# Kernel tuning notes

Hardware: AMD Instinct MI355X
Metric: run time of the kernel (lower is better)

## Reference

```python
import jax, jax.numpy as jnp
import numpy as np

B, N, S, K, R = 4, 8192, 2048, 64, 0.2  # batch, points, centroids, neighbors, ball radius
EPS = 1e-5  # BatchNorm eps


def fps_indices(x, n_samples):
    """Farthest point sampling; returns int32 [B, n_samples] indices."""
    xs = jax.lax.stop_gradient(x)
    Bb, Nn, _ = xs.shape

    def step(carry, _):
        dist, farthest = carry
        centroid = jnp.take_along_axis(xs, farthest[:, None, None], axis=1)  # [B,1,3]
        d = jnp.sum((xs - centroid) ** 2, axis=-1)  # [B,N]
        dist = jnp.minimum(dist, d)
        nxt = jnp.argmax(dist, axis=-1).astype(jnp.int32)
        return (dist, nxt), farthest

    init = (jnp.full((Bb, Nn), 1e10, xs.dtype), jnp.zeros((Bb,), jnp.int32))
    _, idxs = jax.lax.scan(step, init, None, length=n_samples)  # [S,B]
    return jnp.transpose(idxs)  # [B,S]


def ball_query(x, centroids, radius, k):
    """First k point indices within radius of each centroid, -1 padded. int32 [B,S,k]."""
    xs = jax.lax.stop_gradient(x)
    cs = jax.lax.stop_gradient(centroids)
    Nn = xs.shape[1]
    d2 = jnp.sum((cs[:, :, None, :] - xs[:, None, :, :]) ** 2, axis=-1)  # [B,S,N]
    cand = jnp.where(d2 < radius * radius, jnp.arange(Nn, dtype=jnp.int32), Nn)
    neg_topk, _ = jax.lax.top_k(-cand, k)  # k smallest candidate indices
    idx = -neg_topk
    return jnp.where(idx == Nn, -1, idx)


def _forward(x, x_complete, layers, idx_fps, idx_ball):
    centroids = jnp.take_along_axis(x, idx_fps[..., None], axis=1)  # [B,S,3]
    valid = idx_ball >= 0  # [B,S,K]
    sidx = jnp.maximum(idx_ball, 0)
    gather = lambda pts: jax.vmap(lambda p, i: p[i])(pts, sidx)  # [B,S,K,C]
    x_local = gather(x) - centroids[:, :, None, :]  # relative coords
    feats = jnp.concatenate([gather(x_complete), x_local], axis=-1)  # [B,S,K,67]
    h = feats.reshape(B, S * K, -1).transpose(0, 2, 1)  # [B,67,S*K]
    for (W, b, g, bt, m, v) in layers:  # Conv1d(k=1) -> BN(eval) -> ReLU
        h = jnp.einsum('oc,bcn->bon', W, h) + b[None, :, None]
        h = (h - m[None, :, None]) * (g * jax.lax.rsqrt(v + EPS))[None, :, None] + bt[None, :, None]
        h = jax.nn.relu(h)
    h = h.reshape(B, -1, S, K)  # [B,128,S,K]
    h = jnp.where(valid[:, None, :, :], h, -jnp.inf)  # mask invalid neighbors
    pooled = jnp.max(h, axis=3)  # masked max pool over neighborhood
    return centroids, pooled.transpose(0, 2, 1)  # [B,S,3], [B,S,128]


def setup_inputs():
    key = jax.random.key(0)
    ks = jax.random.split(key, 8)
    x = jax.random.uniform(ks[0], (B, N, 3), jnp.float32)
    x_complete = jax.random.normal(ks[1], (B, N, 64), jnp.float32)
    dims = [67, 64, 64, 128]
    inp = {'x': x, 'x_complete': x_complete}
    for i in range(3):
        cin, cout = dims[i], dims[i + 1]
        kk = jax.random.split(ks[2 + i], 6)
        inp[f'W{i+1}'] = jax.random.normal(kk[0], (cout, cin), jnp.float32) * 0.05
        inp[f'b{i+1}'] = jax.random.normal(kk[1], (cout,), jnp.float32) * 0.02
        inp[f'g{i+1}'] = 1.0 + 0.1 * jax.random.normal(kk[2], (cout,), jnp.float32)
        inp[f'bt{i+1}'] = jax.random.normal(kk[3], (cout,), jnp.float32) * 0.02
        inp[f'm{i+1}'] = jax.random.normal(kk[4], (cout,), jnp.float32) * 0.05
        inp[f'v{i+1}'] = jax.random.uniform(kk[5], (cout,), jnp.float32, minval=0.5, maxval=1.5)
    return inp


def reference(x, x_complete, W1, b1, g1, bt1, m1, v1, W2, b2, g2, bt2, m2, v2, W3, b3, g3, bt3, m3, v3):
    idx_fps = fps_indices(x, S)
    cen_sg = jnp.take_along_axis(jax.lax.stop_gradient(x), idx_fps[..., None], axis=1)
    idx_ball = ball_query(x, cen_sg, R, K)
    layers = ((W1, b1, g1, bt1, m1, v1), (W2, b2, g2, bt2, m2, v2), (W3, b3, g3, bt3, m3, v3))
    return _forward(x, x_complete, layers, idx_fps, idx_ball)
```

## Files before the change

### kernel.cpp

```cpp
#include <hip/hip_runtime.h>
#include <math.h>

#define BATCH 4
#define NPTS  8192
#define NSAMP 2048
#define KNBR  64
#define EPSF  1e-5f

typedef float v2f __attribute__((ext_vector_type(2)));

__global__ void prep_kernel(const float* __restrict__ W1, const float* __restrict__ W2,
                            const float* __restrict__ W3,
                            float* __restrict__ W1t, float* __restrict__ W2t,
                            float* __restrict__ W3t) {
    int t = threadIdx.x;
    for (int i = t; i < 64 * 67; i += 256) { int o = i / 67, c = i % 67; W1t[c * 64 + o] = W1[i]; }
    for (int i = t; i < 64 * 64; i += 256) { int o = i >> 6, c = i & 63; W2t[c * 64 + o] = W2[i]; }
    for (int i = t; i < 128 * 64; i += 256) { int o = i >> 6, c = i & 63; W3t[c * 128 + o] = W3[i]; }
}

#define DPP_FMAX(v, ctrl)                                                            \
    do {                                                                             \
        int _t = __builtin_amdgcn_update_dpp(0, __float_as_int(v), ctrl, 0xf, 0xf, true); \
        (v) = fmaxf((v), __int_as_float(_t));                                        \
    } while (0)

__global__ __launch_bounds__(256, 1) void fps_kernel(const float* __restrict__ x,
                                                     float* __restrict__ cen_out) {
#pragma clang fp contract(off)
    const int b = blockIdx.x;
    const int tid = threadIdx.x;
    const int lane = tid & 63;
    const int wid = tid >> 6;
    __shared__ float sx[NPTS], sy[NPTS], sz[NPTS];
    __shared__ __align__(16) float sd[2][4];
    __shared__ __align__(16) int   si[2][4];
    __shared__ int hist[NSAMP];

    const float* xb = x + (size_t)b * NPTS * 3;
    for (int i = tid; i < NPTS; i += 256) {
        sx[i] = xb[3 * i + 0];
        sy[i] = xb[3 * i + 1];
        sz[i] = xb[3 * i + 2];
    }
    __syncthreads();

    v2f px[16], py[16], pz[16], dist[16];
    const int base = tid * 32;
#pragma unroll
    for (int j = 0; j < 16; j++) {
        int p = base + 2 * j;
        px[j] = *(const v2f*)&sx[p];
        py[j] = *(const v2f*)&sy[p];
        pz[j] = *(const v2f*)&sz[p];
        dist[j] = (v2f){1e10f, 1e10f};
    }

    int cur = 0;
    float cx = sx[0], cy = sy[0], cz = sz[0];
    for (int s = 0; s < NSAMP; s++) {
        if (tid == 0) hist[s] = cur;
        const v2f cvx = (v2f){cx, cx}, cvy = (v2f){cy, cy}, cvz = (v2f){cz, cz};
#pragma unroll
        for (int j = 0; j < 16; j++) {
            v2f dx = px[j] - cvx;
            v2f dy = py[j] - cvy;
            v2f dz = pz[j] - cvz;
            v2f d = ((dx * dx) + (dy * dy)) + (dz * dz);
            v2f dm;
            dm.x = fminf(dist[j].x, d.x);
            dm.y = fminf(dist[j].y, d.y);
            dist[j] = dm;
        }
        float t[16];
#pragma unroll
        for (int j = 0; j < 16; j++) t[j] = fmaxf(dist[j].x, dist[j].y);
#pragma unroll
        for (int off = 8; off >= 1; off >>= 1) {
#pragma unroll
            for (int j = 0; j < 8; j++)
                if (j < off) t[j] = fmaxf(t[j], t[j + off]);
        }
        float bestd = t[0];

        float w = bestd;
        DPP_FMAX(w, 0x111);
        DPP_FMAX(w, 0x112);
        DPP_FMAX(w, 0x114);
        DPP_FMAX(w, 0x118);
        DPP_FMAX(w, 0x142);
        DPP_FMAX(w, 0x143);
        const float wmax = __int_as_float(__builtin_amdgcn_readlane(__float_as_int(w), 63));

        unsigned long long mask = __ballot(bestd == wmax);
        int wl = (int)__builtin_ctzll(mask);

        int lj = 0;
#pragma unroll
        for (int j = 15; j >= 0; j--) {
            if (dist[j].y == wmax) lj = 2 * j + 1;
            if (dist[j].x == wmax) lj = 2 * j;
        }
        int widx = __builtin_amdgcn_readlane(base + lj, wl);

        const int p = s & 1;
        if (lane == 0) { sd[p][wid] = wmax; si[p][wid] = widx; }
        __syncthreads();

        float4 dv = *(const float4*)&sd[p][0];
        int4   iv = *(const int4*)&si[p][0];
        float bb = dv.x; int bi = iv.x;
        if (dv.y > bb) { bb = dv.y; bi = iv.y; }
        if (dv.z > bb) { bb = dv.z; bi = iv.z; }
        if (dv.w > bb) { bb = dv.w; bi = iv.w; }
        cur = bi;
        cx = sx[cur]; cy = sy[cur]; cz = sz[cur];
    }

    __syncthreads();
    for (int i = tid; i < NSAMP; i += 256) {
        int idx = hist[i];
        float* o = cen_out + ((size_t)b * NSAMP + i) * 3;
        o[0] = sx[idx]; o[1] = sy[idx]; o[2] = sz[idx];
    }
}

__global__ __launch_bounds__(256) void ball_kernel(const float* __restrict__ x,
                                                   const float* __restrict__ cen,
                                                   int* __restrict__ idxb) {
    const int wid = threadIdx.x >> 6, lane = threadIdx.x & 63;
    const int id = blockIdx.x * 4 + wid;
    const int b = id >> 11;
    const float r2 = (float)(0.2 * 0.2);
    const float cx = cen[3 * id], cy = cen[3 * id + 1], cz = cen[3 * id + 2];
    const float* xb = x + (size_t)b * NPTS * 3;

    int count = 0;
    for (int base = 0; base < NPTS && count < KNBR; base += 64) {
        int p = base + lane;
        float pxv = xb[3 * p], pyv = xb[3 * p + 1], pzv = xb[3 * p + 2];
        float dx = __fsub_rn(cx, pxv);
        float dy = __fsub_rn(cy, pyv);
        float dz = __fsub_rn(cz, pzv);
        float d2 = __fadd_rn(__fadd_rn(__fmul_rn(dx, dx), __fmul_rn(dy, dy)), __fmul_rn(dz, dz));
        bool hit = d2 < r2;
        unsigned long long m = __ballot(hit);
        if (hit) {
            int pos = count + __popcll(m & ((1ull << lane) - 1ull));
            if (pos < KNBR) idxb[(size_t)id * KNBR + pos] = p;
        }
        count += (int)__popcll(m);
    }
    for (int pos = count + lane; pos < KNBR; pos += 64)
        idxb[(size_t)id * KNBR + pos] = -1;
}

__global__ __launch_bounds__(256) void mlp_kernel(
    const float* __restrict__ x, const float* __restrict__ xc,
    const float* __restrict__ cen, const int* __restrict__ idxb,
    const float* __restrict__ W1t, const float* __restrict__ b1, const float* __restrict__ g1,
    const float* __restrict__ bt1, const float* __restrict__ m1, const float* __restrict__ v1,
    const float* __restrict__ W2t, const float* __restrict__ b2, const float* __restrict__ g2,
    const float* __restrict__ bt2, const float* __restrict__ m2, const float* __restrict__ v2,
    const float* __restrict__ W3t, const float* __restrict__ b3, const float* __restrict__ g3,
    const float* __restrict__ bt3, const float* __restrict__ m3, const float* __restrict__ v3,
    float* __restrict__ pooled) {
    const int wid = threadIdx.x >> 6, lane = threadIdx.x & 63;
    const int id = blockIdx.x * 4 + wid;
    const int b = id >> 11;
    __shared__ float sred[4][64][33];

    int il = idxb[(size_t)id * KNBR + lane];
    bool valid = il >= 0;
    int ik = valid ? il : 0;

    float cx = cen[3 * id], cy = cen[3 * id + 1], cz = cen[3 * id + 2];
    const float* xp = x + ((size_t)b * NPTS + ik) * 3;
    const float* xcp = xc + ((size_t)b * NPTS + ik) * 64;

    float h1[64];
#pragma unroll
    for (int o = 0; o < 64; o++) h1[o] = 0.f;
#pragma unroll
    for (int c4 = 0; c4 < 16; c4++) {
        float4 t = ((const float4*)xcp)[c4];
        float tv0 = t.x, tv1 = t.y, tv2 = t.z, tv3 = t.w;
#pragma unroll
        for (int o = 0; o < 64; o++) h1[o] = fmaf(W1t[(c4 * 4 + 0) * 64 + o], tv0, h1[o]);
#pragma unroll
        for (int o = 0; o < 64; o++) h1[o] = fmaf(W1t[(c4 * 4 + 1) * 64 + o], tv1, h1[o]);
#pragma unroll
        for (int o = 0; o < 64; o++) h1[o] = fmaf(W1t[(c4 * 4 + 2) * 64 + o], tv2, h1[o]);
#pragma unroll
        for (int o = 0; o < 64; o++) h1[o] = fmaf(W1t[(c4 * 4 + 3) * 64 + o], tv3, h1[o]);
    }
    {
        float xl0 = xp[0] - cx, xl1 = xp[1] - cy, xl2 = xp[2] - cz;
#pragma unroll
        for (int o = 0; o < 64; o++) h1[o] = fmaf(W1t[64 * 64 + o], xl0, h1[o]);
#pragma unroll
        for (int o = 0; o < 64; o++) h1[o] = fmaf(W1t[65 * 64 + o], xl1, h1[o]);
#pragma unroll
        for (int o = 0; o < 64; o++) h1[o] = fmaf(W1t[66 * 64 + o], xl2, h1[o]);
    }
#pragma unroll
    for (int o = 0; o < 64; o++) {
        float sc = g1[o] * rsqrtf(v1[o] + EPSF);
        h1[o] = fmaxf(fmaf(h1[o] + b1[o] - m1[o], sc, bt1[o]), 0.f);
    }

    float h2[64];
#pragma unroll
    for (int o = 0; o < 64; o++) h2[o] = 0.f;
#pragma unroll
    for (int c = 0; c < 64; c++) {
        float hv = h1[c];
#pragma unroll
        for (int o = 0; o < 64; o++) h2[o] = fmaf(W2t[c * 64 + o], hv, h2[o]);
    }
#pragma unroll
    for (int o = 0; o < 64; o++) {
        float sc = g2[o] * rsqrtf(v2[o] + EPSF);
        h2[o] = fmaxf(fmaf(h2[o] + b2[o] - m2[o], sc, bt2[o]), 0.f);
    }

    for (int ch = 0; ch < 4; ch++) {
        float acc[32];
#pragma unroll
        for (int oo = 0; oo < 32; oo++) acc[oo] = 0.f;
#pragma unroll
        for (int c = 0; c < 64; c++) {
            float hv = h2[c];
#pragma unroll
            for (int oo = 0; oo < 32; oo++)
                acc[oo] = fmaf(W3t[c * 128 + ch * 32 + oo], hv, acc[oo]);
        }
#pragma unroll
        for (int oo = 0; oo < 32; oo++) {
            int o = ch * 32 + oo;
            float sc = g3[o] * rsqrtf(v3[o] + EPSF);
            float t = fmaxf(fmaf(acc[oo] + b3[o] - m3[o], sc, bt3[o]), 0.f);
            sred[wid][lane][oo] = valid ? t : -INFINITY;
        }
        __syncthreads();
        {
            int c = lane & 31, half = lane >> 5;
            float mx = -INFINITY;
#pragma unroll
            for (int r = 0; r < 32; r++) mx = fmaxf(mx, sred[wid][half * 32 + r][c]);
            mx = fmaxf(mx, __shfl_xor(mx, 32, 64));
            if (lane < 32) pooled[(size_t)id * 128 + ch * 32 + c] = mx;
        }
        __syncthreads();
    }
}

extern "C" void kernel_launch(void* const* d_in, const int* in_sizes, int n_in,
                              void* d_out, int out_size, void* d_ws, size_t ws_size,
                              hipStream_t stream) {
    const float* x  = (const float*)d_in[0];
    const float* xc = (const float*)d_in[1];
    const float* W1 = (const float*)d_in[2];
    const float* b1 = (const float*)d_in[3];
    const float* g1 = (const float*)d_in[4];
    const float* bt1 = (const float*)d_in[5];
    const float* m1 = (const float*)d_in[6];
    const float* v1 = (const float*)d_in[7];
    const float* W2 = (const float*)d_in[8];
    const float* b2 = (const float*)d_in[9];
    const float* g2 = (const float*)d_in[10];
    const float* bt2 = (const float*)d_in[11];
    const float* m2 = (const float*)d_in[12];
    const float* v2 = (const float*)d_in[13];
    const float* W3 = (const float*)d_in[14];
    const float* b3 = (const float*)d_in[15];
    const float* g3 = (const float*)d_in[16];
    const float* bt3 = (const float*)d_in[17];
    const float* m3 = (const float*)d_in[18];
    const float* v3 = (const float*)d_in[19];

    float* out = (float*)d_out;
    float* cen = out;
    float* pooled = out + (size_t)BATCH * NSAMP * 3;

    int* idxb = (int*)d_ws;
    float* W1t = (float*)((char*)d_ws + (size_t)BATCH * NSAMP * KNBR * 4);
    float* W2t = W1t + 67 * 64;
    float* W3t = W2t + 64 * 64;

    prep_kernel<<<1, 256, 0, stream>>>(W1, W2, W3, W1t, W2t, W3t);
    fps_kernel<<<BATCH, 256, 0, stream>>>(x, cen);
    ball_kernel<<<(BATCH * NSAMP) / 4, 256, 0, stream>>>(x, cen, idxb);
    mlp_kernel<<<(BATCH * NSAMP) / 4, 256, 0, stream>>>(
        x, xc, cen, idxb,
        W1t, b1, g1, bt1, m1, v1,
        W2t, b2, g2, bt2, m2, v2,
        W3t, b3, g3, bt3, m3, v3,
        pooled);
}
```

Baseline: 2.295 ms.

## Pack FPS distance and index into 64-bit key for single-pass argmax

Replaces the FPS per-step argmax (float max reduction, ballot, then an index search over registers) with one 64-bit key that holds the distance bits in the high word and an inverted index in the low word. The key is reduced with DPP in a single pass. Point coordinates are also stored as float4 in LDS so the next centroid is fetched with one vector load. This shortens the serial per-iteration critical path, but each DPP step now moves two 32-bit halves and does a 64-bit compare.

```diff
diff --git a/kernel.cpp b/kernel.cpp
--- a/kernel.cpp
+++ b/kernel.cpp
@@ -19,10 +19,15 @@
     for (int i = t; i < 128 * 64; i += 256) { int o = i >> 6, c = i & 63; W3t[c * 128 + o] = W3[i]; }
 }
 
-#define DPP_FMAX(v, ctrl)                                                            \
-    do {                                                                             \
-        int _t = __builtin_amdgcn_update_dpp(0, __float_as_int(v), ctrl, 0xf, 0xf, true); \
-        (v) = fmaxf((v), __int_as_float(_t));                                        \
+#define DPP_KMAX(k, ctrl)                                                              \
+    do {                                                                               \
+        unsigned lo_ = (unsigned)(k);                                                  \
+        unsigned hi_ = (unsigned)((k) >> 32);                                          \
+        int slo_ = __builtin_amdgcn_update_dpp(0, (int)lo_, ctrl, 0xf, 0xf, true);     \
+        int shi_ = __builtin_amdgcn_update_dpp(0, (int)hi_, ctrl, 0xf, 0xf, true);     \
+        unsigned long long ks_ =                                                       \
+            ((unsigned long long)(unsigned)shi_ << 32) | (unsigned)slo_;               \
+        if (ks_ > (k)) (k) = ks_;                                                      \
     } while (0)
 
 __global__ __launch_bounds__(256, 1) void fps_kernel(const float* __restrict__ x,
@@ -32,35 +37,35 @@
     const int tid = threadIdx.x;
     const int lane = tid & 63;
     const int wid = tid >> 6;
-    __shared__ float sx[NPTS], sy[NPTS], sz[NPTS];
-    __shared__ __align__(16) float sd[2][4];
-    __shared__ __align__(16) int   si[2][4];
+    __shared__ float4 sp[NPTS];
+    __shared__ __align__(16) unsigned long long pubk[2][4];
     __shared__ int hist[NSAMP];
 
     const float* xb = x + (size_t)b * NPTS * 3;
     for (int i = tid; i < NPTS; i += 256) {
-        sx[i] = xb[3 * i + 0];
-        sy[i] = xb[3 * i + 1];
-        sz[i] = xb[3 * i + 2];
+        sp[i] = (float4){xb[3 * i + 0], xb[3 * i + 1], xb[3 * i + 2], 0.f};
     }
     __syncthreads();
 
     v2f px[16], py[16], pz[16], dist[16];
     const int base = tid * 32;
+    const unsigned nb = 0x7FFFFFFFu - (unsigned)base;
 #pragma unroll
     for (int j = 0; j < 16; j++) {
-        int p = base + 2 * j;
-        px[j] = *(const v2f*)&sx[p];
-        py[j] = *(const v2f*)&sy[p];
-        pz[j] = *(const v2f*)&sz[p];
+        float4 a = sp[base + 2 * j];
+        float4 c = sp[base + 2 * j + 1];
+        px[j] = (v2f){a.x, c.x};
+        py[j] = (v2f){a.y, c.y};
+        pz[j] = (v2f){a.z, c.z};
         dist[j] = (v2f){1e10f, 1e10f};
     }
 
     int cur = 0;
-    float cx = sx[0], cy = sy[0], cz = sz[0];
+    float4 cp = sp[0];
     for (int s = 0; s < NSAMP; s++) {
         if (tid == 0) hist[s] = cur;
-        const v2f cvx = (v2f){cx, cx}, cvy = (v2f){cy, cy}, cvz = (v2f){cz, cz};
+        const v2f cvx = (v2f){cp.x, cp.x}, cvy = (v2f){cp.y, cp.y}, cvz = (v2f){cp.z, cp.z};
+        unsigned long long kacc[4] = {0ull, 0ull, 0ull, 0ull};
 #pragma unroll
         for (int j = 0; j < 16; j++) {
             v2f dx = px[j] - cvx;
@@ -71,57 +76,42 @@
             dm.x = fminf(dist[j].x, d.x);
             dm.y = fminf(dist[j].y, d.y);
             dist[j] = dm;
-        }
-        float t[16];
-#pragma unroll
-        for (int j = 0; j < 16; j++) t[j] = fmaxf(dist[j].x, dist[j].y);
-#pragma unroll
-        for (int off = 8; off >= 1; off >>= 1) {
-#pragma unroll
-            for (int j = 0; j < 8; j++)
-                if (j < off) t[j] = fmaxf(t[j], t[j + off]);
-        }
-        float bestd = t[0];
-
-        float w = bestd;
-        DPP_FMAX(w, 0x111);
-        DPP_FMAX(w, 0x112);
-        DPP_FMAX(w, 0x114);
-        DPP_FMAX(w, 0x118);
-        DPP_FMAX(w, 0x142);
-        DPP_FMAX(w, 0x143);
-        const float wmax = __int_as_float(__builtin_amdgcn_readlane(__float_as_int(w), 63));
-
-        unsigned long long mask = __ballot(bestd == wmax);
-        int wl = (int)__builtin_ctzll(mask);
-
-        int lj = 0;
-#pragma unroll
-        for (int j = 15; j >= 0; j--) {
-            if (dist[j].y == wmax) lj = 2 * j + 1;
-            if (dist[j].x == wmax) lj = 2 * j;
-        }
-        int widx = __builtin_amdgcn_readlane(base + lj, wl);
+            float t = fmaxf(dm.x, dm.y);
+            unsigned so = (dm.x == t) ? (unsigned)(2 * j) : (unsigned)(2 * j + 1);
+            unsigned long long key =
+                ((unsigned long long)__float_as_uint(t) << 32) | (nb - so);
+            if (key > kacc[j & 3]) kacc[j & 3] = key;
+        }
+        unsigned long long ka = kacc[0] > kacc[1] ? kacc[0] : kacc[1];
+        unsigned long long kb = kacc[2] > kacc[3] ? kacc[2] : kacc[3];
+        unsigned long long k = ka > kb ? ka : kb;
+
+        DPP_KMAX(k, 0x111);
+        DPP_KMAX(k, 0x112);
+        DPP_KMAX(k, 0x114);
+        DPP_KMAX(k, 0x118);
+        DPP_KMAX(k, 0x142);
+        DPP_KMAX(k, 0x143);
 
         const int p = s & 1;
-        if (lane == 0) { sd[p][wid] = wmax; si[p][wid] = widx; }
+        if (lane == 63) pubk[p][wid] = k;
         __syncthreads();
 
-        float4 dv = *(const float4*)&sd[p][0];
-        int4   iv = *(const int4*)&si[p][0];
-        float bb = dv.x; int bi = iv.x;
-        if (dv.y > bb) { bb = dv.y; bi = iv.y; }
-        if (dv.z > bb) { bb = dv.z; bi = iv.z; }
-        if (dv.w > bb) { bb = dv.w; bi = iv.w; }
-        cur = bi;
-        cx = sx[cur]; cy = sy[cur]; cz = sz[cur];
+        unsigned long long q0 = pubk[p][0], q1 = pubk[p][1];
+        unsigned long long q2 = pubk[p][2], q3 = pubk[p][3];
+        unsigned long long m0 = q0 > q1 ? q0 : q1;
+        unsigned long long m1 = q2 > q3 ? q2 : q3;
+        unsigned long long kbest = m0 > m1 ? m0 : m1;
+        cur = (int)(0x7FFFFFFFu - (unsigned)kbest);
+        cp = sp[cur];
     }
 
     __syncthreads();
     for (int i = tid; i < NSAMP; i += 256) {
         int idx = hist[i];
+        float4 q = sp[idx];
         float* o = cen_out + ((size_t)b * NSAMP + i) * 3;
-        o[0] = sx[idx]; o[1] = sy[idx]; o[2] = sz[idx];
+        o[0] = q.x; o[1] = q.y; o[2] = q.z;
     }
 }
 
```

New measurement: 2.456 ms. 7.1% more time.

## Fuse FPS, ball query and MLP into persistent kernel with chunked progress flags

Applied to the files above, without the earlier changes.

Merges the three kernels into one persistent kernel of 128 blocks. Four blocks run farthest point sampling and publish centroids in chunks of 64 with a release-ordered progress counter. The other blocks claim work units through atomics, spin until the matching chunk is ready, then run ball query and the MLP. This overlaps the serial FPS phase with the downstream work and drops the idxb round-trip through global memory. In exchange it depends on all blocks being co-resident, uses only 124 worker blocks, and every block carries the large FPS shared-memory footprint, which limits occupancy.

```diff
diff --git a/kernel.cpp b/kernel.cpp
--- a/kernel.cpp
+++ b/kernel.cpp
@@ -6,17 +6,21 @@
 #define NSAMP 2048
 #define KNBR  64
 #define EPSF  1e-5f
+#define CHUNK  64
+#define NCHUNK (NSAMP / CHUNK)
+#define NUNIT  (NCHUNK * BATCH)
 
 typedef float v2f __attribute__((ext_vector_type(2)));
 
 __global__ void prep_kernel(const float* __restrict__ W1, const float* __restrict__ W2,
                             const float* __restrict__ W3,
                             float* __restrict__ W1t, float* __restrict__ W2t,
-                            float* __restrict__ W3t) {
+                            float* __restrict__ W3t, int* __restrict__ cnt) {
     int t = threadIdx.x;
     for (int i = t; i < 64 * 67; i += 256) { int o = i / 67, c = i % 67; W1t[c * 64 + o] = W1[i]; }
     for (int i = t; i < 64 * 64; i += 256) { int o = i >> 6, c = i & 63; W2t[c * 64 + o] = W2[i]; }
     for (int i = t; i < 128 * 64; i += 256) { int o = i >> 6, c = i & 63; W3t[c * 128 + o] = W3[i]; }
+    for (int i = t; i < NUNIT + BATCH; i += 256) cnt[i] = 0;
 }
 
 #define DPP_FMAX(v, ctrl)                                                            \
@@ -25,233 +29,278 @@
         (v) = fmaxf((v), __int_as_float(_t));                                        \
     } while (0)
 
-__global__ __launch_bounds__(256, 1) void fps_kernel(const float* __restrict__ x,
-                                                     float* __restrict__ cen_out) {
-#pragma clang fp contract(off)
-    const int b = blockIdx.x;
-    const int tid = threadIdx.x;
-    const int lane = tid & 63;
-    const int wid = tid >> 6;
-    __shared__ float sx[NPTS], sy[NPTS], sz[NPTS];
-    __shared__ __align__(16) float sd[2][4];
-    __shared__ __align__(16) int   si[2][4];
-    __shared__ int hist[NSAMP];
-
-    const float* xb = x + (size_t)b * NPTS * 3;
-    for (int i = tid; i < NPTS; i += 256) {
-        sx[i] = xb[3 * i + 0];
-        sy[i] = xb[3 * i + 1];
-        sz[i] = xb[3 * i + 2];
-    }
-    __syncthreads();
-
-    v2f px[16], py[16], pz[16], dist[16];
-    const int base = tid * 32;
-#pragma unroll
-    for (int j = 0; j < 16; j++) {
-        int p = base + 2 * j;
-        px[j] = *(const v2f*)&sx[p];
-        py[j] = *(const v2f*)&sy[p];
-        pz[j] = *(const v2f*)&sz[p];
-        dist[j] = (v2f){1e10f, 1e10f};
-    }
-
-    int cur = 0;
-    float cx = sx[0], cy = sy[0], cz = sz[0];
-    for (int s = 0; s < NSAMP; s++) {
-        if (tid == 0) hist[s] = cur;
-        const v2f cvx = (v2f){cx, cx}, cvy = (v2f){cy, cy}, cvz = (v2f){cz, cz};
-#pragma unroll
-        for (int j = 0; j < 16; j++) {
-            v2f dx = px[j] - cvx;
-            v2f dy = py[j] - cvy;
-            v2f dz = pz[j] - cvz;
-            v2f d = ((dx * dx) + (dy * dy)) + (dz * dz);
-            v2f dm;
-            dm.x = fminf(dist[j].x, d.x);
-            dm.y = fminf(dist[j].y, d.y);
-            dist[j] = dm;
-        }
-        float t[16];
-#pragma unroll
-        for (int j = 0; j < 16; j++) t[j] = fmaxf(dist[j].x, dist[j].y);
-#pragma unroll
-        for (int off = 8; off >= 1; off >>= 1) {
-#pragma unroll
-            for (int j = 0; j < 8; j++)
-                if (j < off) t[j] = fmaxf(t[j], t[j + off]);
-        }
-        float bestd = t[0];
-
-        float w = bestd;
-        DPP_FMAX(w, 0x111);
-        DPP_FMAX(w, 0x112);
-        DPP_FMAX(w, 0x114);
-        DPP_FMAX(w, 0x118);
-        DPP_FMAX(w, 0x142);
-        DPP_FMAX(w, 0x143);
-        const float wmax = __int_as_float(__builtin_amdgcn_readlane(__float_as_int(w), 63));
-
-        unsigned long long mask = __ballot(bestd == wmax);
-        int wl = (int)__builtin_ctzll(mask);
-
-        int lj = 0;
-#pragma unroll
-        for (int j = 15; j >= 0; j--) {
-            if (dist[j].y == wmax) lj = 2 * j + 1;
-            if (dist[j].x == wmax) lj = 2 * j;
-        }
-        int widx = __builtin_amdgcn_readlane(base + lj, wl);
-
-        const int p = s & 1;
-        if (lane == 0) { sd[p][wid] = wmax; si[p][wid] = widx; }
-        __syncthreads();
-
-        float4 dv = *(const float4*)&sd[p][0];
-        int4   iv = *(const int4*)&si[p][0];
-        float bb = dv.x; int bi = iv.x;
-        if (dv.y > bb) { bb = dv.y; bi = iv.y; }
-        if (dv.z > bb) { bb = dv.z; bi = iv.z; }
-        if (dv.w > bb) { bb = dv.w; bi = iv.w; }
-        cur = bi;
-        cx = sx[cur]; cy = sy[cur]; cz = sz[cur];
-    }
-
-    __syncthreads();
-    for (int i = tid; i < NSAMP; i += 256) {
-        int idx = hist[i];
-        float* o = cen_out + ((size_t)b * NSAMP + i) * 3;
-        o[0] = sx[idx]; o[1] = sy[idx]; o[2] = sz[idx];
-    }
-}
-
-__global__ __launch_bounds__(256) void ball_kernel(const float* __restrict__ x,
-                                                   const float* __restrict__ cen,
-                                                   int* __restrict__ idxb) {
-    const int wid = threadIdx.x >> 6, lane = threadIdx.x & 63;
-    const int id = blockIdx.x * 4 + wid;
-    const int b = id >> 11;
-    const float r2 = (float)(0.2 * 0.2);
-    const float cx = cen[3 * id], cy = cen[3 * id + 1], cz = cen[3 * id + 2];
-    const float* xb = x + (size_t)b * NPTS * 3;
-
-    int count = 0;
-    for (int base = 0; base < NPTS && count < KNBR; base += 64) {
-        int p = base + lane;
-        float pxv = xb[3 * p], pyv = xb[3 * p + 1], pzv = xb[3 * p + 2];
-        float dx = __fsub_rn(cx, pxv);
-        float dy = __fsub_rn(cy, pyv);
-        float dz = __fsub_rn(cz, pzv);
-        float d2 = __fadd_rn(__fadd_rn(__fmul_rn(dx, dx), __fmul_rn(dy, dy)), __fmul_rn(dz, dz));
-        bool hit = d2 < r2;
-        unsigned long long m = __ballot(hit);
-        if (hit) {
-            int pos = count + __popcll(m & ((1ull << lane) - 1ull));
-            if (pos < KNBR) idxb[(size_t)id * KNBR + pos] = p;
-        }
-        count += (int)__popcll(m);
-    }
-    for (int pos = count + lane; pos < KNBR; pos += 64)
-        idxb[(size_t)id * KNBR + pos] = -1;
-}
-
-__global__ __launch_bounds__(256) void mlp_kernel(
+__global__ __launch_bounds__(256, 1) void mega_kernel(
     const float* __restrict__ x, const float* __restrict__ xc,
-    const float* __restrict__ cen, const int* __restrict__ idxb,
+    float* __restrict__ cen, float* __restrict__ pooled,
     const float* __restrict__ W1t, const float* __restrict__ b1, const float* __restrict__ g1,
     const float* __restrict__ bt1, const float* __restrict__ m1, const float* __restrict__ v1,
     const float* __restrict__ W2t, const float* __restrict__ b2, const float* __restrict__ g2,
     const float* __restrict__ bt2, const float* __restrict__ m2, const float* __restrict__ v2,
     const float* __restrict__ W3t, const float* __restrict__ b3, const float* __restrict__ g3,
     const float* __restrict__ bt3, const float* __restrict__ m3, const float* __restrict__ v3,
-    float* __restrict__ pooled) {
-    const int wid = threadIdx.x >> 6, lane = threadIdx.x & 63;
-    const int id = blockIdx.x * 4 + wid;
-    const int b = id >> 11;
+    int* __restrict__ cnt) {
+#pragma clang fp contract(off)
+    const int tid = threadIdx.x;
+    const int lane = tid & 63;
+    const int wid = tid >> 6;
+
+    __shared__ float sx[NPTS], sy[NPTS], sz[NPTS];
+    __shared__ int hist[NSAMP];
+    __shared__ __align__(16) float sd[2][4];
+    __shared__ __align__(16) int   si[2][4];
     __shared__ float sred[4][64][33];
-
-    int il = idxb[(size_t)id * KNBR + lane];
-    bool valid = il >= 0;
-    int ik = valid ? il : 0;
-
-    float cx = cen[3 * id], cy = cen[3 * id + 1], cz = cen[3 * id + 2];
-    const float* xp = x + ((size_t)b * NPTS + ik) * 3;
-    const float* xcp = xc + ((size_t)b * NPTS + ik) * 64;
-
-    float h1[64];
-#pragma unroll
-    for (int o = 0; o < 64; o++) h1[o] = 0.f;
-#pragma unroll
-    for (int c4 = 0; c4 < 16; c4++) {
-        float4 t = ((const float4*)xcp)[c4];
-        float tv0 = t.x, tv1 = t.y, tv2 = t.z, tv3 = t.w;
-#pragma unroll
-        for (int o = 0; o < 64; o++) h1[o] = fmaf(W1t[(c4 * 4 + 0) * 64 + o], tv0, h1[o]);
-#pragma unroll
-        for (int o = 0; o < 64; o++) h1[o] = fmaf(W1t[(c4 * 4 + 1) * 64 + o], tv1, h1[o]);
-#pragma unroll
-        for (int o = 0; o < 64; o++) h1[o] = fmaf(W1t[(c4 * 4 + 2) * 64 + o], tv2, h1[o]);
-#pragma unroll
-        for (int o = 0; o < 64; o++) h1[o] = fmaf(W1t[(c4 * 4 + 3) * 64 + o], tv3, h1[o]);
+    __shared__ int widx[4][64];
+    __shared__ int sflag, sclaim;
+
+    int* claim = cnt;
+    int* prog  = cnt + NUNIT;
+
+    if (blockIdx.x < BATCH) {
+        const int b = blockIdx.x;
+        const float* xb = x + (size_t)b * NPTS * 3;
+        for (int i = tid; i < NPTS; i += 256) {
+            sx[i] = xb[3 * i + 0];
+            sy[i] = xb[3 * i + 1];
+            sz[i] = xb[3 * i + 2];
+        }
+        __syncthreads();
+
+        v2f px[16], py[16], pz[16], dist[16];
+        const int base = tid * 32;
+#pragma unroll
+        for (int j = 0; j < 16; j++) {
+            int p = base + 2 * j;
+            px[j] = *(const v2f*)&sx[p];
+            py[j] = *(const v2f*)&sy[p];
+            pz[j] = *(const v2f*)&sz[p];
+            dist[j] = (v2f){1e10f, 1e10f};
+        }
+
+        int cur = 0;
+        float cx = sx[0], cy = sy[0], cz = sz[0];
+        for (int s = 0; s < NSAMP; s++) {
+            if (tid == 0) hist[s] = cur;
+            const v2f cvx = (v2f){cx, cx}, cvy = (v2f){cy, cy}, cvz = (v2f){cz, cz};
+#pragma unroll
+            for (int j = 0; j < 16; j++) {
+                v2f dx = px[j] - cvx;
+                v2f dy = py[j] - cvy;
+                v2f dz = pz[j] - cvz;
+                v2f d = ((dx * dx) + (dy * dy)) + (dz * dz);
+                v2f dm;
+                dm.x = fminf(dist[j].x, d.x);
+                dm.y = fminf(dist[j].y, d.y);
+                dist[j] = dm;
+            }
+            float t[16];
+#pragma unroll
+            for (int j = 0; j < 16; j++) t[j] = fmaxf(dist[j].x, dist[j].y);
+#pragma unroll
+            for (int off = 8; off >= 1; off >>= 1) {
+#pragma unroll
+                for (int j = 0; j < 8; j++)
+                    if (j < off) t[j] = fmaxf(t[j], t[j + off]);
+            }
+            float bestd = t[0];
+
+            float w = bestd;
+            DPP_FMAX(w, 0x111);
+            DPP_FMAX(w, 0x112);
+            DPP_FMAX(w, 0x114);
+            DPP_FMAX(w, 0x118);
+            DPP_FMAX(w, 0x142);
+            DPP_FMAX(w, 0x143);
+            const float wmax = __int_as_float(__builtin_amdgcn_readlane(__float_as_int(w), 63));
+
+            unsigned long long mask = __ballot(bestd == wmax);
+            int wl = (int)__builtin_ctzll(mask);
+
+            int lj = 0;
+#pragma unroll
+            for (int j = 15; j >= 0; j--) {
+                if (dist[j].y == wmax) lj = 2 * j + 1;
+                if (dist[j].x == wmax) lj = 2 * j;
+            }
+            int widx2 = __builtin_amdgcn_readlane(base + lj, wl);
+
+            const int p = s & 1;
+            if (lane == 0) { sd[p][wid] = wmax; si[p][wid] = widx2; }
+            __syncthreads();
+
+            float4 dv = *(const float4*)&sd[p][0];
+            int4   iv = *(const int4*)&si[p][0];
+            float bb = dv.x; int bi = iv.x;
+            if (dv.y > bb) { bb = dv.y; bi = iv.y; }
+            if (dv.z > bb) { bb = dv.z; bi = iv.z; }
+            if (dv.w > bb) { bb = dv.w; bi = iv.w; }
+            cur = bi;
+            cx = sx[cur]; cy = sy[cur]; cz = sz[cur];
+
+            if ((s & (CHUNK - 1)) == (CHUNK - 1)) {
+                int c = s >> 6;
+                if (tid < 3 * CHUNK) {
+                    int i = (c << 6) + tid / 3;
+                    int f = tid - 3 * (tid / 3);
+                    int h = hist[i];
+                    float vv = (f == 0) ? sx[h] : (f == 1) ? sy[h] : sz[h];
+                    __hip_atomic_store(&cen[((size_t)b * NSAMP + i) * 3 + f], vv,
+                                       __ATOMIC_RELAXED, __HIP_MEMORY_SCOPE_AGENT);
+                }
+                __syncthreads();
+                if (tid == 0)
+                    __hip_atomic_store(&prog[b], s + 1,
+                                       __ATOMIC_RELEASE, __HIP_MEMORY_SCOPE_AGENT);
+            }
+        }
+        return;
     }
-    {
-        float xl0 = xp[0] - cx, xl1 = xp[1] - cy, xl2 = xp[2] - cz;
-#pragma unroll
-        for (int o = 0; o < 64; o++) h1[o] = fmaf(W1t[64 * 64 + o], xl0, h1[o]);
-#pragma unroll
-        for (int o = 0; o < 64; o++) h1[o] = fmaf(W1t[65 * 64 + o], xl1, h1[o]);
-#pragma unroll
-        for (int o = 0; o < 64; o++) h1[o] = fmaf(W1t[66 * 64 + o], xl2, h1[o]);
-    }
-#pragma unroll
-    for (int o = 0; o < 64; o++) {
-        float sc = g1[o] * rsqrtf(v1[o] + EPSF);
-        h1[o] = fmaxf(fmaf(h1[o] + b1[o] - m1[o], sc, bt1[o]), 0.f);
-    }
-
-    float h2[64];
-#pragma unroll
-    for (int o = 0; o < 64; o++) h2[o] = 0.f;
-#pragma unroll
-    for (int c = 0; c < 64; c++) {
-        float hv = h1[c];
-#pragma unroll
-        for (int o = 0; o < 64; o++) h2[o] = fmaf(W2t[c * 64 + o], hv, h2[o]);
-    }
-#pragma unroll
-    for (int o = 0; o < 64; o++) {
-        float sc = g2[o] * rsqrtf(v2[o] + EPSF);
-        h2[o] = fmaxf(fmaf(h2[o] + b2[o] - m2[o], sc, bt2[o]), 0.f);
-    }
-
-    for (int ch = 0; ch < 4; ch++) {
-        float acc[32];
-#pragma unroll
-        for (int oo = 0; oo < 32; oo++) acc[oo] = 0.f;
-#pragma unroll
-        for (int c = 0; c < 64; c++) {
-            float hv = h2[c];
-#pragma unroll
-            for (int oo = 0; oo < 32; oo++)
-                acc[oo] = fmaf(W3t[c * 128 + ch * 32 + oo], hv, acc[oo]);
-        }
-#pragma unroll
-        for (int oo = 0; oo < 32; oo++) {
-            int o = ch * 32 + oo;
-            float sc = g3[o] * rsqrtf(v3[o] + EPSF);
-            float t = fmaxf(fmaf(acc[oo] + b3[o] - m3[o], sc, bt3[o]), 0.f);
-            sred[wid][lane][oo] = valid ? t : -INFINITY;
-        }
+
+    const float r2 = (float)(0.2 * 0.2);
+    for (int u = 0; u < NUNIT; u++) {
+        const int c = u >> 2, bb = u & 3;
+        const int target = (c + 1) * CHUNK;
+
+        if (tid == 0)
+            sflag = (__hip_atomic_load(&claim[u], __ATOMIC_RELAXED,
+                                       __HIP_MEMORY_SCOPE_AGENT) < CHUNK) ? 1 : 0;
         __syncthreads();
-        {
-            int c = lane & 31, half = lane >> 5;
-            float mx = -INFINITY;
-#pragma unroll
-            for (int r = 0; r < 32; r++) mx = fmaxf(mx, sred[wid][half * 32 + r][c]);
-            mx = fmaxf(mx, __shfl_xor(mx, 32, 64));
-            if (lane < 32) pooled[(size_t)id * 128 + ch * 32 + c] = mx;
-        }
+        int enter = sflag;
         __syncthreads();
+        if (!enter) continue;
+
+        int guard = 0;
+        while (true) {
+            if (tid == 0) {
+                int pv = __hip_atomic_load(&prog[bb], __ATOMIC_ACQUIRE,
+                                           __HIP_MEMORY_SCOPE_AGENT);
+                guard++;
+                sflag = (pv >= target || guard > (1 << 21)) ? 1 : 0;
+            }
+            __syncthreads();
+            int ok = sflag;
+            __syncthreads();
+            if (ok) break;
+            __builtin_amdgcn_s_sleep(32);
+        }
+
+        while (true) {
+            if (tid == 0) sclaim = atomicAdd(&claim[u], 4);
+            __syncthreads();
+            int it = sclaim;
+            __syncthreads();
+            if (it >= CHUNK) break;
+            const int sidx = (c << 6) + it + wid;
+
+            const float* xb2 = x + (size_t)bb * NPTS * 3;
+            size_t co = ((size_t)bb * NSAMP + sidx) * 3;
+            float ccx = __hip_atomic_load(&cen[co + 0], __ATOMIC_RELAXED, __HIP_MEMORY_SCOPE_AGENT);
+            float ccy = __hip_atomic_load(&cen[co + 1], __ATOMIC_RELAXED, __HIP_MEMORY_SCOPE_AGENT);
+            float ccz = __hip_atomic_load(&cen[co + 2], __ATOMIC_RELAXED, __HIP_MEMORY_SCOPE_AGENT);
+
+            widx[wid][lane] = -1;
+            __syncthreads();
+            int count = 0;
+            for (int bse = 0; bse < NPTS && count < KNBR; bse += 64) {
+                int p = bse + lane;
+                float pxv = xb2[3 * p], pyv = xb2[3 * p + 1], pzv = xb2[3 * p + 2];
+                float dx = __fsub_rn(ccx, pxv);
+                float dy = __fsub_rn(ccy, pyv);
+                float dz = __fsub_rn(ccz, pzv);
+                float d2 = __fadd_rn(__fadd_rn(__fmul_rn(dx, dx), __fmul_rn(dy, dy)),
+                                     __fmul_rn(dz, dz));
+                bool hit = d2 < r2;
+                unsigned long long m = __ballot(hit);
+                if (hit) {
+                    int pos = count + __popcll(m & ((1ull << lane) - 1ull));
+                    if (pos < KNBR) widx[wid][pos] = p;
+                }
+                count += (int)__popcll(m);
+            }
+            __syncthreads();
+            int il = widx[wid][lane];
+            bool valid = il >= 0;
+            int ik = valid ? il : 0;
+
+            const float* xp  = x  + ((size_t)bb * NPTS + ik) * 3;
+            const float* xcp = xc + ((size_t)bb * NPTS + ik) * 64;
+
+            float h1[64];
+#pragma unroll
+            for (int o = 0; o < 64; o++) h1[o] = 0.f;
+#pragma unroll
+            for (int c4 = 0; c4 < 16; c4++) {
+                float4 t = ((const float4*)xcp)[c4];
+                float tv0 = t.x, tv1 = t.y, tv2 = t.z, tv3 = t.w;
+#pragma unroll
+                for (int o = 0; o < 64; o++) h1[o] = fmaf(W1t[(c4 * 4 + 0) * 64 + o], tv0, h1[o]);
+#pragma unroll
+                for (int o = 0; o < 64; o++) h1[o] = fmaf(W1t[(c4 * 4 + 1) * 64 + o], tv1, h1[o]);
+#pragma unroll
+                for (int o = 0; o < 64; o++) h1[o] = fmaf(W1t[(c4 * 4 + 2) * 64 + o], tv2, h1[o]);
+#pragma unroll
+                for (int o = 0; o < 64; o++) h1[o] = fmaf(W1t[(c4 * 4 + 3) * 64 + o], tv3, h1[o]);
+            }
+            {
+                float xl0 = xp[0] - ccx, xl1 = xp[1] - ccy, xl2 = xp[2] - ccz;
+#pragma unroll
+                for (int o = 0; o < 64; o++) h1[o] = fmaf(W1t[64 * 64 + o], xl0, h1[o]);
+#pragma unroll
+                for (int o = 0; o < 64; o++) h1[o] = fmaf(W1t[65 * 64 + o], xl1, h1[o]);
+#pragma unroll
+                for (int o = 0; o < 64; o++) h1[o] = fmaf(W1t[66 * 64 + o], xl2, h1[o]);
+            }
+#pragma unroll
+            for (int o = 0; o < 64; o++) {
+                float sc = g1[o] * rsqrtf(v1[o] + EPSF);
+                h1[o] = fmaxf(fmaf(h1[o] + b1[o] - m1[o], sc, bt1[o]), 0.f);
+            }
+
+            float h2[64];
+#pragma unroll
+            for (int o = 0; o < 64; o++) h2[o] = 0.f;
+#pragma unroll
+            for (int cc2 = 0; cc2 < 64; cc2++) {
+                float hv = h1[cc2];
+#pragma unroll
+                for (int o = 0; o < 64; o++) h2[o] = fmaf(W2t[cc2 * 64 + o], hv, h2[o]);
+            }
+#pragma unroll
+            for (int o = 0; o < 64; o++) {
+                float sc = g2[o] * rsqrtf(v2[o] + EPSF);
+                h2[o] = fmaxf(fmaf(h2[o] + b2[o] - m2[o], sc, bt2[o]), 0.f);
+            }
+
+            for (int ch = 0; ch < 4; ch++) {
+                float acc[32];
+#pragma unroll
+                for (int oo = 0; oo < 32; oo++) acc[oo] = 0.f;
+#pragma unroll
+                for (int cc2 = 0; cc2 < 64; cc2++) {
+                    float hv = h2[cc2];
+#pragma unroll
+                    for (int oo = 0; oo < 32; oo++)
+                        acc[oo] = fmaf(W3t[cc2 * 128 + ch * 32 + oo], hv, acc[oo]);
+                }
+#pragma unroll
+                for (int oo = 0; oo < 32; oo++) {
+                    int o = ch * 32 + oo;
+                    float sc = g3[o] * rsqrtf(v3[o] + EPSF);
+                    float t = fmaxf(fmaf(acc[oo] + b3[o] - m3[o], sc, bt3[o]), 0.f);
+                    sred[wid][lane][oo] = valid ? t : -INFINITY;
+                }
+                __syncthreads();
+                {
+                    int cc3 = lane & 31, half = lane >> 5;
+                    float mx = -INFINITY;
+#pragma unroll
+                    for (int r = 0; r < 32; r++) mx = fmaxf(mx, sred[wid][half * 32 + r][cc3]);
+                    mx = fmaxf(mx, __shfl_xor(mx, 32, 64));
+                    if (lane < 32)
+                        pooled[((size_t)bb * NSAMP + sidx) * 128 + ch * 32 + cc3] = mx;
+                }
+                __syncthreads();
+            }
+        }
     }
 }
 
@@ -283,18 +332,16 @@
     float* cen = out;
     float* pooled = out + (size_t)BATCH * NSAMP * 3;
 
-    int* idxb = (int*)d_ws;
+    int* cnt = (int*)d_ws;
     float* W1t = (float*)((char*)d_ws + (size_t)BATCH * NSAMP * KNBR * 4);
     float* W2t = W1t + 67 * 64;
     float* W3t = W2t + 64 * 64;
 
-    prep_kernel<<<1, 256, 0, stream>>>(W1, W2, W3, W1t, W2t, W3t);
-    fps_kernel<<<BATCH, 256, 0, stream>>>(x, cen);
-    ball_kernel<<<(BATCH * NSAMP) / 4, 256, 0, stream>>>(x, cen, idxb);
-    mlp_kernel<<<(BATCH * NSAMP) / 4, 256, 0, stream>>>(
-        x, xc, cen, idxb,
+    prep_kernel<<<1, 256, 0, stream>>>(W1, W2, W3, W1t, W2t, W3t, cnt);
+    mega_kernel<<<128, 256, 0, stream>>>(
+        x, xc, cen, pooled,
         W1t, b1, g1, bt1, m1, v1,
         W2t, b2, g2, bt2, m2, v2,
         W3t, b3, g3, bt3, m3, v3,
-        pooled);
+        cnt);
 }
```

Result: slower. 2.398 ms (+4.5%).
